# Kernel optimization log

Hardware: AMD Instinct MI355X
Metric: run time of the kernel (lower is better)

## Reference

```python
import jax, jax.numpy as jnp
import numpy as np

DN = ('NCDHW', 'OIDHW', 'NCDHW')  # conv dimension numbers for 3D conv in torch layout
EPS = 1e-14


def setup_inputs() -> dict:
    key = jax.random.key(0)
    k1, k2 = jax.random.split(key)
    # xs: [B, C, D, H, W]
    xs = jax.random.normal(k1, (16, 128, 24, 24, 24), dtype=jnp.float32)
    # feature_vectors (prototypes): [num_features, C, w_1, h_1, L_1]
    feature_vectors = jax.random.normal(k2, (128, 128, 3, 3, 3), dtype=jnp.float32)
    return {"xs": xs, "feature_vectors": feature_vectors}


def reference(xs, feature_vectors):
    F_, C, kd, kh, kw = feature_vectors.shape
    # ||x_patch||^2: the original convolves xs**2 with all-ones weights of shape
    # [F, C, kd, kh, kw], producing F identical channels. We compute a single
    # sum-pool channel (same math) and let broadcasting supply the F channels.
    ones = jnp.ones((1, C, kd, kh, kw), dtype=xs.dtype)
    xs_squared_l2 = jax.lax.conv_general_dilated(
        xs * xs, ones, window_strides=(1, 1, 1), padding='VALID',
        dimension_numbers=DN)  # [B, 1, D', H', W']
    # ||p||^2 per prototype: [F, 1, 1, 1]
    ps_squared_l2 = jnp.sum(feature_vectors * feature_vectors,
                            axis=(1, 2, 3, 4)).reshape(-1, 1, 1, 1)
    # <x_patch, p>: the real weighted conv. [B, F, D', H', W']
    xs_conv = jax.lax.conv_general_dilated(
        xs, feature_vectors, window_strides=(1, 1, 1), padding='VALID',
        dimension_numbers=DN)
    distance = xs_squared_l2 + ps_squared_l2 - 2.0 * xs_conv
    return jnp.sqrt(jnp.abs(distance) + EPS)
```

## Files before the change

### kernel.cpp

```cpp
#include <hip/hip_runtime.h>
#include <hip/hip_bf16.h>

typedef __attribute__((ext_vector_type(8))) __bf16 bf16x8;
typedef __attribute__((ext_vector_type(2))) __bf16 bf16x2;
typedef __attribute__((ext_vector_type(4))) float f32x4;

#define B_   16
#define C_   128
#define DIM  24
#define F_   128
#define OD   22
#define OS   (OD*OD*OD)
#define SPB  (DIM*DIM*DIM)
#define K_   3456
#define M_   (B_*OS)
#define OUTN (B_*F_*OS)
#define NMT  666

__device__ __forceinline__ void async16(const void* g, void* l) {
  __builtin_amdgcn_global_load_lds(
      (const __attribute__((address_space(1))) unsigned int*)g,
      (__attribute__((address_space(3))) unsigned int*)l, 16, 0, 0);
}

__device__ __constant__ int DOFF[27] = {
    0,    1,    2,    24,   25,   26,   48,   49,   50,
    576,  577,  578,  600,  601,  602,  624,  625,  626,
    1152, 1153, 1154, 1176, 1177, 1178, 1200, 1201, 1202};

__global__ __launch_bounds__(256) void prep_x(const float* __restrict__ xs,
                                              __bf16* __restrict__ xt,
                                              float* __restrict__ s1) {
  __shared__ float tile[C_ * 97];
  __shared__ float red[192];
  const int blk = blockIdx.x;
  const int yg = blk % 6;
  const int t2 = blk / 6;
  const int z = t2 % DIM;
  const int b = t2 / DIM;
  const int t = threadIdx.x;
  const float* src = xs + (size_t)b * C_ * SPB + z * (DIM * DIM) + yg * 96;
  for (int it = 0; it < 12; ++it) {
    int idx = it * 256 + t;
    int c = idx / 24, f4 = idx - c * 24;
    const float4 v = *(const float4*)(src + (size_t)c * SPB + f4 * 4);
    float* d = &tile[c * 97 + f4 * 4];
    d[0] = v.x; d[1] = v.y; d[2] = v.z; d[3] = v.w;
  }
  __syncthreads();
  size_t obase = ((size_t)b * SPB + z * (DIM * DIM) + yg * 96) * C_;
  for (int it = 0; it < 24; ++it) {
    int idx = it * 256 + t;
    int c2 = idx & 63, x = idx >> 6;
    bf16x2 v;
    v[0] = (__bf16)tile[(2 * c2) * 97 + x];
    v[1] = (__bf16)tile[(2 * c2 + 1) * 97 + x];
    *(bf16x2*)&xt[obase + (size_t)x * C_ + 2 * c2] = v;
  }
  if (t < 192) {
    int g = t / 96, p = t - g * 96;
    float s = 0.f;
    for (int c = g; c < C_; c += 2) {
      float v = tile[c * 97 + p];
      s += v * v;
    }
    red[g * 96 + p] = s;
  }
  __syncthreads();
  if (t < 96)
    s1[((size_t)b * SPB + z * (DIM * DIM) + yg * 96) + t] = red[t] + red[96 + t];
}

__global__ __launch_bounds__(256) void pool_prepw(
    const float* __restrict__ s1, float* __restrict__ xsq,
    const float* __restrict__ fv, __bf16* __restrict__ Wt,
    float* __restrict__ psq) {
  if (blockIdx.x >= NMT) {
    __shared__ float tile[K_];
    const int f = blockIdx.x - NMT;
    const float* src = fv + (size_t)f * K_;
    float part = 0.f;
    for (int idx = threadIdx.x; idx < K_; idx += 256) {
      float v = src[idx];
      tile[idx] = v;
      part += v * v;
    }
    __syncthreads();
    for (int idx = threadIdx.x; idx < K_; idx += 256) {
      int c = idx & 127, off = idx >> 7;
      Wt[(size_t)f * K_ + idx] = (__bf16)tile[c * 27 + off];
    }
    for (int o = 32; o > 0; o >>= 1) part += __shfl_down(part, o, 64);
    __shared__ float red[4];
    int w = threadIdx.x >> 6, l = threadIdx.x & 63;
    if (l == 0) red[w] = part;
    __syncthreads();
    if (threadIdx.x == 0) psq[f] = red[0] + red[1] + red[2] + red[3];
    return;
  }
  int i = blockIdx.x * 256 + threadIdx.x;
  if (i >= M_) return;
  int ow = i % OD;
  int t = i / OD;
  int oh = t % OD; t /= OD;
  int od = t % OD;
  int b = t / OD;
  const float* p = s1 + ((b * DIM + od) * DIM + oh) * DIM + ow;
  float s = 0.f;
#pragma unroll
  for (int dz = 0; dz < 3; ++dz)
#pragma unroll
    for (int dy = 0; dy < 3; ++dy)
#pragma unroll
      for (int dx = 0; dx < 3; ++dx)
        s += p[dz * 576 + dy * 24 + dx];
  xsq[i] = s;
}

__global__ __launch_bounds__(256, 2) void l2gemm(
    const __bf16* __restrict__ xt, const __bf16* __restrict__ Wt,
    const float* __restrict__ xsq, const float* __restrict__ psq,
    float* __restrict__ out) {
  __shared__ __align__(16) __bf16 Wl[128 * 64];
  __shared__ __align__(16) __bf16 Pl[256 * 64];
  const int mt = (blockIdx.x & 7) * 84 + (blockIdx.x >> 3);
  if (mt >= NMT) return;
  const int t = threadIdx.x;
  const int l = t & 63, w = t >> 6;
  const int quad = l >> 4, lan = l & 15;
  const int e = t & 7, r0 = t >> 3;
  const int esw = (e ^ (r0 & 7)) * 8;

  int sb[8];
#pragma unroll
  for (int p = 0; p < 8; ++p) {
    int m = mt * 256 + r0 + 32 * p;
    if (m >= M_) m = M_ - 1;
    int b = m / OS;
    int s = m - b * OS;
    int od = s / (OD * OD);
    int s2 = s - od * (OD * OD);
    int oh = s2 / OD;
    int ow = s2 - oh * OD;
    sb[p] = b * SPB + od * 576 + oh * 24 + ow;
  }

  f32x4 acc[4][8];
#pragma unroll
  for (int i = 0; i < 4; ++i)
#pragma unroll
    for (int n = 0; n < 8; ++n) acc[i][n] = (f32x4){0.f, 0.f, 0.f, 0.f};

  const int wm = (w >> 1) * 64;
  const int wn = (w & 1) * 128;
  __bf16* wl_base = &Wl[(w * 8) * 64];
  __bf16* pl_base = &Pl[(w * 8) * 64];

#pragma unroll 1
  for (int kt = 0; kt < 54; ++kt) {
    int doff = DOFF[kt >> 1];
    int c0 = (kt & 1) << 6;
    __syncthreads();
#pragma unroll
    for (int p = 0; p < 8; ++p) {
      const __bf16* gp = xt + (((size_t)(sb[p] + doff)) << 7) + c0 + esw;
      async16(gp, pl_base + (size_t)(32 * p) * 64);
    }
#pragma unroll
    for (int p = 0; p < 4; ++p) {
      const __bf16* gw = Wt + (size_t)(r0 + 32 * p) * K_ + kt * 64 + esw;
      async16(gw, wl_base + (size_t)(32 * p) * 64);
    }
    __syncthreads();
#pragma unroll
    for (int kk = 0; kk < 2; ++kk) {
      bf16x8 a[4], bb[8];
      const int swz = (((kk * 4 + quad) ^ (lan & 7))) * 8;
#pragma unroll
      for (int i = 0; i < 4; ++i)
        a[i] = *(const bf16x8*)&Wl[(wm + i * 16 + lan) * 64 + swz];
#pragma unroll
      for (int n = 0; n < 8; ++n)
        bb[n] = *(const bf16x8*)&Pl[(wn + n * 16 + lan) * 64 + swz];
#pragma unroll
      for (int i = 0; i < 4; ++i)
#pragma unroll
        for (int n = 0; n < 8; ++n)
          acc[i][n] = __builtin_amdgcn_mfma_f32_16x16x32_bf16(a[i], bb[n],
                                                              acc[i][n], 0, 0, 0);
    }
  }

  int mb[8];
  float xv[8];
  bool ok[8];
#pragma unroll
  for (int n = 0; n < 8; ++n) {
    int m = mt * 256 + wn + n * 16 + lan;
    ok[n] = (m < M_);
    int mc = ok[n] ? m : (M_ - 1);
    int b = mc / OS;
    int s = mc - b * OS;
    mb[n] = b * (F_ * OS) + s;
    xv[n] = xsq[mc];
  }
#pragma unroll
  for (int i = 0; i < 4; ++i) {
#pragma unroll
    for (int r = 0; r < 4; ++r) {
      int f = wm + i * 16 + quad * 4 + r;
      float pq = psq[f];
#pragma unroll
      for (int n = 0; n < 8; ++n) {
        if (ok[n]) {
          float d = xv[n] + pq - 2.0f * acc[i][n][r];
          out[mb[n] + f * OS] = sqrtf(fabsf(d) + 1e-14f);
        }
      }
    }
  }
}

__global__ void l2conv_direct(const float* __restrict__ xs,
                              const float* __restrict__ fv,
                              float* __restrict__ out) {
  int i = blockIdx.x * 256 + threadIdx.x;
  if (i >= OUTN) return;
  int s = i % OS;
  int t2 = i / OS;
  int f = t2 & 127;
  int b = t2 >> 7;
  int od = s / (OD * OD);
  int s2 = s - od * (OD * OD);
  int oh = s2 / OD;
  int ow = s2 - oh * OD;
  const float* xp = xs + (size_t)b * C_ * SPB + od * 576 + oh * 24 + ow;
  const float* wp = fv + (size_t)f * K_;
  float dot = 0.f, xq = 0.f, pq = 0.f;
  for (int c = 0; c < C_; ++c) {
    const float* xpc = xp + (size_t)c * SPB;
    const float* wpc = wp + c * 27;
#pragma unroll
    for (int o = 0; o < 27; ++o) {
      int dz = o / 9;
      int ry = o - dz * 9;
      int dy = ry / 3;
      int dx = ry - dy * 3;
      float xv = xpc[dz * 576 + dy * 24 + dx];
      float wv = wpc[o];
      dot += xv * wv;
      xq += xv * xv;
      pq += wv * wv;
    }
  }
  out[i] = sqrtf(fabsf(xq + pq - 2.f * dot) + 1e-14f);
}

extern "C" void kernel_launch(void* const* d_in, const int* in_sizes, int n_in,
                              void* d_out, int out_size, void* d_ws,
                              size_t ws_size, hipStream_t stream) {
  const float* xs = (const float*)d_in[0];
  const float* fv = (const float*)d_in[1];
  float* out = (float*)d_out;

  const size_t xt_b  = (size_t)B_ * SPB * C_ * 2;
  const size_t wt_b  = (size_t)F_ * K_ * 2;
  const size_t s1_b  = (size_t)B_ * SPB * 4;
  const size_t xsq_b = (size_t)M_ * 4;
  const size_t psq_b = 512;
  if (ws_size < xt_b + wt_b + s1_b + xsq_b + psq_b) {
    l2conv_direct<<<(OUTN + 255) / 256, 256, 0, stream>>>(xs, fv, out);
    return;
  }
  char* p = (char*)d_ws;
  __bf16* xt = (__bf16*)p;          p += xt_b;
  __bf16* Wt = (__bf16*)p;          p += wt_b;
  float*  s1 = (float*)p;           p += s1_b;
  float*  xsq = (float*)p;          p += xsq_b;
  float*  psq = (float*)p;

  prep_x<<<B_ * DIM * DIM / 4, 256, 0, stream>>>(xs, xt, s1);
  pool_prepw<<<NMT + 128, 256, 0, stream>>>(s1, xsq, fv, Wt, psq);
  l2gemm<<<672, 256, 0, stream>>>(xt, Wt, xsq, psq, out);
}
```

Measured before the change: 412.9 us.

## Load activation fragments directly to registers and double-buffer weights in LDS

The GEMM no longer stages the im2col activation tile in shared memory. Each wave now owns 64 output rows across all 128 filters and loads its B fragments straight from global memory into registers, prefetching the next k-step's fragment. Weights are double-buffered in LDS with async loads, so there is one barrier per iteration instead of two. This trades LDS traffic and sync stalls for uncoalesced-ish global loads, higher register pressure (8x4 accumulators plus fragments), and drops the block-index swizzle.

New measurement: 473.5 us. 14.7% more time.

```diff
diff --git a/kernel.cpp b/kernel.cpp
--- a/kernel.cpp
+++ b/kernel.cpp
@@ -121,20 +121,18 @@
     const __bf16* __restrict__ xt, const __bf16* __restrict__ Wt,
     const float* __restrict__ xsq, const float* __restrict__ psq,
     float* __restrict__ out) {
-  __shared__ __align__(16) __bf16 Wl[128 * 64];
-  __shared__ __align__(16) __bf16 Pl[256 * 64];
-  const int mt = (blockIdx.x & 7) * 84 + (blockIdx.x >> 3);
-  if (mt >= NMT) return;
+  __shared__ __align__(16) __bf16 Wl[2][128 * 64];
   const int t = threadIdx.x;
   const int l = t & 63, w = t >> 6;
   const int quad = l >> 4, lan = l & 15;
   const int e = t & 7, r0 = t >> 3;
   const int esw = (e ^ (r0 & 7)) * 8;
-
-  int sb[8];
-#pragma unroll
-  for (int p = 0; p < 8; ++p) {
-    int m = mt * 256 + r0 + 32 * p;
+  const int mt = blockIdx.x;
+
+  const __bf16* bp[4];
+#pragma unroll
+  for (int n = 0; n < 4; ++n) {
+    int m = mt * 256 + w * 64 + n * 16 + lan;
     if (m >= M_) m = M_ - 1;
     int b = m / OS;
     int s = m - b * OS;
@@ -142,61 +140,72 @@
     int s2 = s - od * (OD * OD);
     int oh = s2 / OD;
     int ow = s2 - oh * OD;
-    sb[p] = b * SPB + od * 576 + oh * 24 + ow;
-  }
-
-  f32x4 acc[4][8];
-#pragma unroll
-  for (int i = 0; i < 4; ++i)
-#pragma unroll
-    for (int n = 0; n < 8; ++n) acc[i][n] = (f32x4){0.f, 0.f, 0.f, 0.f};
-
-  const int wm = (w >> 1) * 64;
-  const int wn = (w & 1) * 128;
-  __bf16* wl_base = &Wl[(w * 8) * 64];
-  __bf16* pl_base = &Pl[(w * 8) * 64];
+    bp[n] = xt + (((size_t)(b * SPB + od * 576 + oh * 24 + ow)) << 7) + quad * 8;
+  }
+
+  f32x4 acc[8][4];
+#pragma unroll
+  for (int i = 0; i < 8; ++i)
+#pragma unroll
+    for (int n = 0; n < 4; ++n) acc[i][n] = (f32x4){0.f, 0.f, 0.f, 0.f};
+
+#pragma unroll
+  for (int p = 0; p < 4; ++p)
+    async16(Wt + (size_t)(r0 + 32 * p) * K_ + esw, &Wl[0][(w * 8 + 32 * p) * 64]);
+  bf16x8 bb0[4];
+#pragma unroll
+  for (int n = 0; n < 4; ++n) bb0[n] = *(const bf16x8*)(bp[n]);
 
 #pragma unroll 1
   for (int kt = 0; kt < 54; ++kt) {
-    int doff = DOFF[kt >> 1];
-    int c0 = (kt & 1) << 6;
+    const __bf16* wcur = Wl[kt & 1];
     __syncthreads();
-#pragma unroll
-    for (int p = 0; p < 8; ++p) {
-      const __bf16* gp = xt + (((size_t)(sb[p] + doff)) << 7) + c0 + esw;
-      async16(gp, pl_base + (size_t)(32 * p) * 64);
-    }
-#pragma unroll
-    for (int p = 0; p < 4; ++p) {
-      const __bf16* gw = Wt + (size_t)(r0 + 32 * p) * K_ + kt * 64 + esw;
-      async16(gw, wl_base + (size_t)(32 * p) * 64);
-    }
-    __syncthreads();
-#pragma unroll
-    for (int kk = 0; kk < 2; ++kk) {
-      bf16x8 a[4], bb[8];
-      const int swz = (((kk * 4 + quad) ^ (lan & 7))) * 8;
-#pragma unroll
-      for (int i = 0; i < 4; ++i)
-        a[i] = *(const bf16x8*)&Wl[(wm + i * 16 + lan) * 64 + swz];
-#pragma unroll
-      for (int n = 0; n < 8; ++n)
-        bb[n] = *(const bf16x8*)&Pl[(wn + n * 16 + lan) * 64 + swz];
-#pragma unroll
-      for (int i = 0; i < 4; ++i)
-#pragma unroll
-        for (int n = 0; n < 8; ++n)
-          acc[i][n] = __builtin_amdgcn_mfma_f32_16x16x32_bf16(a[i], bb[n],
-                                                              acc[i][n], 0, 0, 0);
-    }
-  }
-
-  int mb[8];
-  float xv[8];
-  bool ok[8];
-#pragma unroll
-  for (int n = 0; n < 8; ++n) {
-    int m = mt * 256 + wn + n * 16 + lan;
+    if (kt < 53) {
+#pragma unroll
+      for (int p = 0; p < 4; ++p)
+        async16(Wt + (size_t)(r0 + 32 * p) * K_ + (kt + 1) * 64 + esw,
+                &Wl[(kt + 1) & 1][(w * 8 + 32 * p) * 64]);
+    }
+    const int doff = DOFF[kt >> 1];
+    const int c0 = (kt & 1) << 6;
+    bf16x8 bb1[4];
+#pragma unroll
+    for (int n = 0; n < 4; ++n)
+      bb1[n] = *(const bf16x8*)(bp[n] + ((size_t)doff << 7) + c0 + 32);
+    bf16x8 a[8];
+#pragma unroll
+    for (int i = 0; i < 8; ++i)
+      a[i] = *(const bf16x8*)&wcur[(i * 16 + lan) * 64 + ((quad) ^ (lan & 7)) * 8];
+#pragma unroll
+    for (int i = 0; i < 8; ++i)
+#pragma unroll
+      for (int n = 0; n < 4; ++n)
+        acc[i][n] = __builtin_amdgcn_mfma_f32_16x16x32_bf16(a[i], bb0[n],
+                                                            acc[i][n], 0, 0, 0);
+    if (kt < 53) {
+      const int doff2 = DOFF[(kt + 1) >> 1];
+      const int c02 = ((kt + 1) & 1) << 6;
+#pragma unroll
+      for (int n = 0; n < 4; ++n)
+        bb0[n] = *(const bf16x8*)(bp[n] + ((size_t)doff2 << 7) + c02);
+    }
+#pragma unroll
+    for (int i = 0; i < 8; ++i)
+      a[i] = *(const bf16x8*)&wcur[(i * 16 + lan) * 64 + ((4 + quad) ^ (lan & 7)) * 8];
+#pragma unroll
+    for (int i = 0; i < 8; ++i)
+#pragma unroll
+      for (int n = 0; n < 4; ++n)
+        acc[i][n] = __builtin_amdgcn_mfma_f32_16x16x32_bf16(a[i], bb1[n],
+                                                            acc[i][n], 0, 0, 0);
+  }
+
+  int mb[4];
+  float xv[4];
+  bool ok[4];
+#pragma unroll
+  for (int n = 0; n < 4; ++n) {
+    int m = mt * 256 + w * 64 + n * 16 + lan;
     ok[n] = (m < M_);
     int mc = ok[n] ? m : (M_ - 1);
     int b = mc / OS;
@@ -205,13 +214,13 @@
     xv[n] = xsq[mc];
   }
 #pragma unroll
-  for (int i = 0; i < 4; ++i) {
+  for (int i = 0; i < 8; ++i) {
 #pragma unroll
     for (int r = 0; r < 4; ++r) {
-      int f = wm + i * 16 + quad * 4 + r;
+      int f = i * 16 + quad * 4 + r;
       float pq = psq[f];
 #pragma unroll
-      for (int n = 0; n < 8; ++n) {
+      for (int n = 0; n < 4; ++n) {
         if (ok[n]) {
           float d = xv[n] + pq - 2.0f * acc[i][n][r];
           out[mb[n] + f * OS] = sqrtf(fabsf(d) + 1e-14f);
@@ -281,5 +290,5 @@
 
   prep_x<<<B_ * DIM * DIM / 4, 256, 0, stream>>>(xs, xt, s1);
   pool_prepw<<<NMT + 128, 256, 0, stream>>>(s1, xsq, fv, Wt, psq);
-  l2gemm<<<672, 256, 0, stream>>>(xt, Wt, xsq, psq, out);
-}
+  l2gemm<<<NMT, 256, 0, stream>>>(xt, Wt, xsq, psq, out);
+}
```
